# Kernel tuning notes

Hardware: AMD Instinct MI355X
Metric: run time of the kernel (lower is better)

Reference implementation:

```python
import jax, jax.numpy as jnp
import numpy as np

FEATURE_MAPS = 128
POOLING_OUT = 4
KERNAL_LEN = 3
EMB_DIM = 300
CLASSES = 7
B, L, N = 64, 512, 2048


def setup_inputs() -> dict:
    key = jax.random.key(0)
    ks = jax.random.split(key, 10)
    sentence = jax.random.normal(ks[0], (B, 1, L, EMB_DIM), dtype=jnp.float32)
    # ROIs: [x1, x2) spans within [0, L], span length in [1, 32]
    x1 = jax.random.randint(ks[1], (N,), 0, L - 33)
    span = jax.random.randint(ks[2], (N,), 1, 33)
    rois = jnp.stack([x1, x1 + span], axis=1).astype(jnp.int64)
    ridx = jax.random.randint(ks[3], (N,), 0, B).astype(jnp.int64)
    s = 0.02
    conv_w = jax.random.normal(ks[4], (FEATURE_MAPS, 1, KERNAL_LEN, EMB_DIM), dtype=jnp.float32) * s
    conv_b = jax.random.normal(ks[5], (FEATURE_MAPS,), dtype=jnp.float32) * s
    FF = FEATURE_MAPS * POOLING_OUT
    fc1_w = jax.random.normal(ks[6], (FF, FF), dtype=jnp.float32) * s
    fc1_b = jax.random.normal(ks[7], (FF,), dtype=jnp.float32) * s
    cls_w = jax.random.normal(ks[8], (CLASSES + 1, FF), dtype=jnp.float32) * s
    cls_b = jax.random.normal(ks[9], (CLASSES + 1,), dtype=jnp.float32) * s
    return {"sentence": sentence, "rois": rois, "ridx": ridx,
            "conv_w": conv_w, "conv_b": conv_b, "fc1_w": fc1_w, "fc1_b": fc1_b,
            "cls_w": cls_w, "cls_b": cls_b}


def reference(sentence, rois, ridx, conv_w, conv_b, fc1_w, fc1_b, cls_w, cls_b):
    # conv1: Conv2d(1->F, (K, D), padding=(1,0)) + ReLU -> [B, F, L, 1]
    feat = jax.lax.conv_general_dilated(
        sentence, conv_w, window_strides=(1, 1),
        padding=((1, 1), (0, 0)),
        dimension_numbers=("NCHW", "OIHW", "NCHW"))
    feat = jax.nn.relu(feat + conv_b[None, :, None, None])[..., 0]  # [B, F, L]
    # ROI max-pool over each span [x1, x2) of the length dim (vectorized)
    g = feat[ridx]                                  # [N, F, L]
    pos = jnp.arange(feat.shape[-1])
    mask = (pos[None, :] >= rois[:, 0:1]) & (pos[None, :] < rois[:, 1:2])  # [N, L]
    neg = jnp.finfo(feat.dtype).min
    pooled = jnp.max(jnp.where(mask[:, None, :], g, neg), axis=-1)  # [N, F]
    # AdaptiveMaxPool2d((1, P)) with input width 1 replicates each channel P times,
    # and .view flattening is channel-major -> jnp.repeat along last axis matches.
    x = jnp.repeat(pooled, POOLING_OUT, axis=-1)    # [N, F*P]
    x = x @ fc1_w.T + fc1_b
    return x @ cls_w.T + cls_b                      # [N, CLASSES+1]
```

## Files before the change

### kernel.cpp

```cpp
#include <hip/hip_runtime.h>
#include <hip/hip_bf16.h>

#define FMAPS 128
#define SEQL  512
#define BATCH 64
#define EMB   300
#define EMBP  320
#define LPAD  514
#define NKC   30
#define NROI  2048
#define FFDIM 512
#define NCLS  8

typedef short bf16x8 __attribute__((ext_vector_type(8)));
typedef float f32x4  __attribute__((ext_vector_type(4)));

static __device__ __forceinline__ float relu_(float x) { return x > 0.f ? x : 0.f; }
static __device__ __forceinline__ ushort bf16bits(float f) {
    __hip_bfloat16 h = __float2bfloat16(f);
    return *reinterpret_cast<ushort*>(&h);
}

__global__ void pad_bf16(const float* __restrict__ x, ushort* __restrict__ xp) {
    const int ROW4 = EMBP / 4;
    int idx = blockIdx.x * blockDim.x + threadIdx.x;
    int total = BATCH * LPAD * ROW4;
    if (idx >= total) return;
    int d4 = idx % ROW4;
    int t  = idx / ROW4;
    int r  = t % LPAD;
    int b  = t / LPAD;
    float4 v = make_float4(0.f, 0.f, 0.f, 0.f);
    if (r >= 1 && r <= SEQL && d4 < (EMB / 4)) {
        v = ((const float4*)(x + ((size_t)(b * SEQL + (r - 1))) * EMB))[d4];
    }
    ushort4 o;
    o.x = bf16bits(v.x); o.y = bf16bits(v.y); o.z = bf16bits(v.z); o.w = bf16bits(v.w);
    ((ushort4*)xp)[idx] = o;
}

__global__ void wpad_frag(const float* __restrict__ cw, ushort* __restrict__ wf) {
    int idx = blockIdx.x * blockDim.x + threadIdx.x;
    if (idx >= NKC * 8 * 64 * 8) return;
    int j    = idx & 7;
    int lane = (idx >> 3) & 63;
    int nt   = (idx >> 9) & 7;
    int kc   = idx >> 12;
    int f = nt * 16 + (lane & 15);
    int k = kc * 32 + (lane >> 4) * 8 + j;
    int kr = k / EMBP, d = k % EMBP;
    float v = (d < EMB) ? cw[f * 900 + kr * 300 + d] : 0.f;
    wf[idx] = bf16bits(v);
}

__global__ void prep_kernel(const float* __restrict__ cls_w,
                            const float* __restrict__ fc1_b,
                            const float* __restrict__ cls_b,
                            float* __restrict__ Mf, float* __restrict__ b2) {
    int t = threadIdx.x;
    Mf[t] = 0.f; Mf[t + 512] = 0.f;
    int c = t >> 6, lane = t & 63;
    float s = 0.f;
    for (int i = lane; i < FFDIM; i += 64)
        s = fmaf(cls_w[c * FFDIM + i], fc1_b[i], s);
#pragma unroll
    for (int off = 32; off; off >>= 1) s += __shfl_xor(s, off, 64);
    if (lane == 0) b2[c] = s + cls_b[c];
}

__global__ void collapse_kernel(const float* __restrict__ cls_w,
                                const float* __restrict__ fc1_w,
                                float* __restrict__ Mf) {
    int f  = threadIdx.x & 127;
    int c0 = (threadIdx.x >> 7) * 4;
    int i0 = blockIdx.x * 16;
    float acc[4] = {0.f, 0.f, 0.f, 0.f};
    for (int i = i0; i < i0 + 16; ++i) {
        float4 w4 = *(const float4*)(fc1_w + (size_t)i * FFDIM + f * 4);
        float ws = (w4.x + w4.y) + (w4.z + w4.w);
#pragma unroll
        for (int cc = 0; cc < 4; ++cc)
            acc[cc] = fmaf(cls_w[(c0 + cc) * FFDIM + i], ws, acc[cc]);
    }
#pragma unroll
    for (int cc = 0; cc < 4; ++cc)
        atomicAdd(Mf + (c0 + cc) * FMAPS + f, acc[cc]);
}

__global__ __launch_bounds__(256, 2) void conv_mfma(
    const ushort* __restrict__ xp, const ushort* __restrict__ wf,
    const float* __restrict__ cb, float* __restrict__ feat) {
    const int t    = threadIdx.x;
    const int lane = t & 63;
    const int wid  = t >> 6;
    const int wm   = wid & 1;
    const int wn   = wid >> 1;
    const int b    = blockIdx.x >> 3;
    const int l0   = (blockIdx.x & 7) << 6;

    const int mrow = lane & 15;
    const int koct = lane >> 4;

    f32x4 acc[2][4] = {};

    const ushort* xrow0 = xp + ((size_t)b * LPAD + (l0 + wm * 32 + mrow)) * EMBP + koct * 8;
    const ushort* wlane = wf + (size_t)(wn * 4) * 512 + (size_t)lane * 8;

#pragma unroll
    for (int kr = 0; kr < 3; ++kr) {
        const ushort* xr = xrow0 + (size_t)kr * EMBP;
#pragma unroll
        for (int dc = 0; dc < 10; ++dc) {
            const int kc = kr * 10 + dc;
            bf16x8 a0 = *(const bf16x8*)(xr + dc * 32);
            bf16x8 a1 = *(const bf16x8*)(xr + 16 * EMBP + dc * 32);
            const ushort* wk = wlane + (size_t)kc * 4096;
            bf16x8 b0 = *(const bf16x8*)(wk);
            bf16x8 b1 = *(const bf16x8*)(wk + 512);
            bf16x8 b2v = *(const bf16x8*)(wk + 1024);
            bf16x8 b3 = *(const bf16x8*)(wk + 1536);
            acc[0][0] = __builtin_amdgcn_mfma_f32_16x16x32_bf16(a0, b0,  acc[0][0], 0, 0, 0);
            acc[0][1] = __builtin_amdgcn_mfma_f32_16x16x32_bf16(a0, b1,  acc[0][1], 0, 0, 0);
            acc[0][2] = __builtin_amdgcn_mfma_f32_16x16x32_bf16(a0, b2v, acc[0][2], 0, 0, 0);
            acc[0][3] = __builtin_amdgcn_mfma_f32_16x16x32_bf16(a0, b3,  acc[0][3], 0, 0, 0);
            acc[1][0] = __builtin_amdgcn_mfma_f32_16x16x32_bf16(a1, b0,  acc[1][0], 0, 0, 0);
            acc[1][1] = __builtin_amdgcn_mfma_f32_16x16x32_bf16(a1, b1,  acc[1][1], 0, 0, 0);
            acc[1][2] = __builtin_amdgcn_mfma_f32_16x16x32_bf16(a1, b2v, acc[1][2], 0, 0, 0);
            acc[1][3] = __builtin_amdgcn_mfma_f32_16x16x32_bf16(a1, b3,  acc[1][3], 0, 0, 0);
        }
    }

#pragma unroll
    for (int n = 0; n < 4; ++n) {
        const int f = wn * 64 + n * 16 + mrow;
        const float bias = cb[f];
#pragma unroll
        for (int m = 0; m < 2; ++m) {
            const int lbase = l0 + wm * 32 + m * 16 + koct * 4;
#pragma unroll
            for (int r = 0; r < 4; ++r) {
                float v = acc[m][n][r] + bias;
                feat[((size_t)b * SEQL + (lbase + r)) * FMAPS + f] = relu_(v);
            }
        }
    }
}

__global__ __launch_bounds__(256) void roi_fc(
    const float* __restrict__ feat, const int* __restrict__ rois,
    const int* __restrict__ ridx, const float* __restrict__ mf,
    const float* __restrict__ b2, float* __restrict__ out) {
    const int w    = threadIdx.x >> 6;
    const int lane = threadIdx.x & 63;
    const int n    = blockIdx.x * 4 + w;
    const int x1 = rois[n * 2 + 0];
    const int x2 = rois[n * 2 + 1];
    const int bi = ridx[n];
    const float* base = feat + ((size_t)bi * SEQL) * FMAPS;
    float m0 = -1e30f, m1 = -1e30f;
    for (int l = x1; l < x2; ++l) {
        const float* row = base + (size_t)l * FMAPS;
        m0 = fmaxf(m0, row[lane]);
        m1 = fmaxf(m1, row[lane + 64]);
    }
    float res[8];
#pragma unroll
    for (int c = 0; c < 8; ++c) {
        float p = m0 * mf[c * FMAPS + lane] + m1 * mf[c * FMAPS + 64 + lane];
#pragma unroll
        for (int off = 32; off; off >>= 1) p += __shfl_xor(p, off, 64);
        res[c] = p;
    }
    if (lane == 0) {
#pragma unroll
        for (int c = 0; c < 8; ++c) out[n * NCLS + c] = res[c] + b2[c];
    }
}

extern "C" void kernel_launch(void* const* d_in, const int* in_sizes, int n_in,
                              void* d_out, int out_size, void* d_ws, size_t ws_size,
                              hipStream_t stream) {
    const float* sentence = (const float*)d_in[0];
    const int*   rois     = (const int*)d_in[1];
    const int*   ridx     = (const int*)d_in[2];
    const float* conv_w   = (const float*)d_in[3];
    const float* conv_b   = (const float*)d_in[4];
    const float* fc1_w    = (const float*)d_in[5];
    const float* fc1_b    = (const float*)d_in[6];
    const float* cls_w    = (const float*)d_in[7];
    const float* cls_b    = (const float*)d_in[8];
    float* out = (float*)d_out;

    char* ws = (char*)d_ws;
    ushort* Xp = (ushort*)ws;
    ushort* Wf = (ushort*)(ws + 21053440);
    float*  Ft = (float*)(ws + 21053440 + 245760);
    float*  Mf = (float*)(ws + 21053440 + 245760 + 16777216);
    float*  b2 = Mf + 1024;

    const int padTotal = BATCH * LPAD * (EMBP / 4);
    hipLaunchKernelGGL(pad_bf16, dim3((padTotal + 255) / 256), dim3(256), 0, stream,
                       sentence, Xp);
    hipLaunchKernelGGL(wpad_frag, dim3((NKC * 8 * 64 * 8) / 256), dim3(256), 0, stream,
                       conv_w, Wf);
    hipLaunchKernelGGL(prep_kernel, dim3(1), dim3(512), 0, stream,
                       cls_w, fc1_b, cls_b, Mf, b2);
    hipLaunchKernelGGL(collapse_kernel, dim3(32), dim3(256), 0, stream,
                       cls_w, fc1_w, Mf);
    hipLaunchKernelGGL(conv_mfma, dim3((BATCH * SEQL) / 64), dim3(256), 0, stream,
                       Xp, Wf, conv_b, Ft);
    hipLaunchKernelGGL(roi_fc, dim3(NROI / 4), dim3(256), 0, stream,
                       Ft, rois, ridx, Mf, b2, out);
}
```

Measured before the change: 140.1 us.

## Fuse preprocessing kernels into one launch and widen conv blocks to 512 threads

Merges the four preprocessing kernels (input pad/convert, weight fragment packing, fc collapse, bias fold) into one launch that dispatches on block index. The collapse step now computes each class row in a single block with a shared-memory reduction instead of zero-initialising and using atomics. The conv kernel moves to 8 waves per block, each holding a 2x2 tile of accumulators instead of 2x4, so it uses fewer registers per wave and can keep more waves resident, at the cost of more A-operand loads per MFMA.

```diff
diff --git a/kernel.cpp b/kernel.cpp
--- a/kernel.cpp
+++ b/kernel.cpp
@@ -12,6 +12,11 @@
 #define FFDIM 512
 #define NCLS  8
 
+#define PAD_BLOCKS  10280
+#define WPAD_BLOCKS 480
+#define MF_BLOCKS   8
+#define B2_BLOCKS   1
+
 typedef short bf16x8 __attribute__((ext_vector_type(8)));
 typedef float f32x4  __attribute__((ext_vector_type(4)));
 
@@ -21,90 +26,95 @@
     return *reinterpret_cast<ushort*>(&h);
 }
 
-__global__ void pad_bf16(const float* __restrict__ x, ushort* __restrict__ xp) {
-    const int ROW4 = EMBP / 4;
-    int idx = blockIdx.x * blockDim.x + threadIdx.x;
-    int total = BATCH * LPAD * ROW4;
-    if (idx >= total) return;
-    int d4 = idx % ROW4;
-    int t  = idx / ROW4;
-    int r  = t % LPAD;
-    int b  = t / LPAD;
-    float4 v = make_float4(0.f, 0.f, 0.f, 0.f);
-    if (r >= 1 && r <= SEQL && d4 < (EMB / 4)) {
-        v = ((const float4*)(x + ((size_t)(b * SEQL + (r - 1))) * EMB))[d4];
-    }
-    ushort4 o;
-    o.x = bf16bits(v.x); o.y = bf16bits(v.y); o.z = bf16bits(v.z); o.w = bf16bits(v.w);
-    ((ushort4*)xp)[idx] = o;
-}
-
-__global__ void wpad_frag(const float* __restrict__ cw, ushort* __restrict__ wf) {
-    int idx = blockIdx.x * blockDim.x + threadIdx.x;
-    if (idx >= NKC * 8 * 64 * 8) return;
-    int j    = idx & 7;
-    int lane = (idx >> 3) & 63;
-    int nt   = (idx >> 9) & 7;
-    int kc   = idx >> 12;
-    int f = nt * 16 + (lane & 15);
-    int k = kc * 32 + (lane >> 4) * 8 + j;
-    int kr = k / EMBP, d = k % EMBP;
-    float v = (d < EMB) ? cw[f * 900 + kr * 300 + d] : 0.f;
-    wf[idx] = bf16bits(v);
-}
-
-__global__ void prep_kernel(const float* __restrict__ cls_w,
-                            const float* __restrict__ fc1_b,
-                            const float* __restrict__ cls_b,
-                            float* __restrict__ Mf, float* __restrict__ b2) {
-    int t = threadIdx.x;
-    Mf[t] = 0.f; Mf[t + 512] = 0.f;
-    int c = t >> 6, lane = t & 63;
-    float s = 0.f;
-    for (int i = lane; i < FFDIM; i += 64)
-        s = fmaf(cls_w[c * FFDIM + i], fc1_b[i], s);
-#pragma unroll
-    for (int off = 32; off; off >>= 1) s += __shfl_xor(s, off, 64);
-    if (lane == 0) b2[c] = s + cls_b[c];
-}
-
-__global__ void collapse_kernel(const float* __restrict__ cls_w,
-                                const float* __restrict__ fc1_w,
-                                float* __restrict__ Mf) {
-    int f  = threadIdx.x & 127;
-    int c0 = (threadIdx.x >> 7) * 4;
-    int i0 = blockIdx.x * 16;
-    float acc[4] = {0.f, 0.f, 0.f, 0.f};
-    for (int i = i0; i < i0 + 16; ++i) {
-        float4 w4 = *(const float4*)(fc1_w + (size_t)i * FFDIM + f * 4);
-        float ws = (w4.x + w4.y) + (w4.z + w4.w);
-#pragma unroll
-        for (int cc = 0; cc < 4; ++cc)
-            acc[cc] = fmaf(cls_w[(c0 + cc) * FFDIM + i], ws, acc[cc]);
-    }
-#pragma unroll
-    for (int cc = 0; cc < 4; ++cc)
-        atomicAdd(Mf + (c0 + cc) * FMAPS + f, acc[cc]);
-}
-
-__global__ __launch_bounds__(256, 2) void conv_mfma(
+__global__ __launch_bounds__(256) void prep_fused(
+    const float* __restrict__ x, const float* __restrict__ conv_w,
+    const float* __restrict__ cls_w, const float* __restrict__ fc1_w,
+    const float* __restrict__ fc1_b, const float* __restrict__ cls_b,
+    ushort* __restrict__ xp, ushort* __restrict__ wf,
+    float* __restrict__ Mf, float* __restrict__ b2) {
+    __shared__ float red[2][128];
+    const int tid = threadIdx.x;
+    int blk = blockIdx.x;
+
+    if (blk < PAD_BLOCKS) {
+        const int ROW4 = EMBP / 4;
+        int idx = blk * 256 + tid;
+        int d4 = idx % ROW4;
+        int t  = idx / ROW4;
+        int r  = t % LPAD;
+        int b  = t / LPAD;
+        float4 v = make_float4(0.f, 0.f, 0.f, 0.f);
+        if (r >= 1 && r <= SEQL && d4 < (EMB / 4)) {
+            v = ((const float4*)(x + ((size_t)(b * SEQL + (r - 1))) * EMB))[d4];
+        }
+        ushort4 o;
+        o.x = bf16bits(v.x); o.y = bf16bits(v.y); o.z = bf16bits(v.z); o.w = bf16bits(v.w);
+        ((ushort4*)xp)[idx] = o;
+        return;
+    }
+    blk -= PAD_BLOCKS;
+
+    if (blk < WPAD_BLOCKS) {
+        int idx = blk * 256 + tid;
+        int j    = idx & 7;
+        int lane = (idx >> 3) & 63;
+        int nt   = (idx >> 9) & 7;
+        int kc   = idx >> 12;
+        int f = nt * 16 + (lane & 15);
+        int k = kc * 32 + (lane >> 4) * 8 + j;
+        int kr = k / EMBP, d = k % EMBP;
+        float v = (d < EMB) ? conv_w[f * 900 + kr * 300 + d] : 0.f;
+        wf[idx] = bf16bits(v);
+        return;
+    }
+    blk -= WPAD_BLOCKS;
+
+    if (blk < MF_BLOCKS) {
+        const int c = blk;
+        const int g = tid & 127;
+        const int q = tid >> 7;
+        float s = 0.f;
+        for (int i = q * 256; i < q * 256 + 256; ++i) {
+            float4 w4 = *(const float4*)(fc1_w + (size_t)i * FFDIM + 4 * g);
+            float ws = (w4.x + w4.y) + (w4.z + w4.w);
+            s = fmaf(cls_w[c * FFDIM + i], ws, s);
+        }
+        red[q][g] = s;
+        __syncthreads();
+        if (tid < 128) Mf[c * FMAPS + tid] = red[0][tid] + red[1][tid];
+        return;
+    }
+
+    {
+        const int c = tid >> 5;
+        const int l32 = tid & 31;
+        float s = 0.f;
+        for (int i = l32; i < FFDIM; i += 32)
+            s = fmaf(cls_w[c * FFDIM + i], fc1_b[i], s);
+#pragma unroll
+        for (int off = 16; off; off >>= 1) s += __shfl_xor(s, off, 64);
+        if (l32 == 0) b2[c] = s + cls_b[c];
+    }
+}
+
+__global__ __launch_bounds__(512, 4) void conv_mfma(
     const ushort* __restrict__ xp, const ushort* __restrict__ wf,
     const float* __restrict__ cb, float* __restrict__ feat) {
     const int t    = threadIdx.x;
     const int lane = t & 63;
     const int wid  = t >> 6;
-    const int wm   = wid & 1;
-    const int wn   = wid >> 1;
+    const int wm   = wid >> 2;
+    const int wn   = wid & 3;
     const int b    = blockIdx.x >> 3;
     const int l0   = (blockIdx.x & 7) << 6;
 
     const int mrow = lane & 15;
     const int koct = lane >> 4;
 
-    f32x4 acc[2][4] = {};
+    f32x4 acc[2][2] = {};
 
     const ushort* xrow0 = xp + ((size_t)b * LPAD + (l0 + wm * 32 + mrow)) * EMBP + koct * 8;
-    const ushort* wlane = wf + (size_t)(wn * 4) * 512 + (size_t)lane * 8;
+    const ushort* wlane = wf + (size_t)(wn * 2) * 512 + (size_t)lane * 8;
 
 #pragma unroll
     for (int kr = 0; kr < 3; ++kr) {
@@ -117,22 +127,16 @@
             const ushort* wk = wlane + (size_t)kc * 4096;
             bf16x8 b0 = *(const bf16x8*)(wk);
             bf16x8 b1 = *(const bf16x8*)(wk + 512);
-            bf16x8 b2v = *(const bf16x8*)(wk + 1024);
-            bf16x8 b3 = *(const bf16x8*)(wk + 1536);
-            acc[0][0] = __builtin_amdgcn_mfma_f32_16x16x32_bf16(a0, b0,  acc[0][0], 0, 0, 0);
-            acc[0][1] = __builtin_amdgcn_mfma_f32_16x16x32_bf16(a0, b1,  acc[0][1], 0, 0, 0);
-            acc[0][2] = __builtin_amdgcn_mfma_f32_16x16x32_bf16(a0, b2v, acc[0][2], 0, 0, 0);
-            acc[0][3] = __builtin_amdgcn_mfma_f32_16x16x32_bf16(a0, b3,  acc[0][3], 0, 0, 0);
-            acc[1][0] = __builtin_amdgcn_mfma_f32_16x16x32_bf16(a1, b0,  acc[1][0], 0, 0, 0);
-            acc[1][1] = __builtin_amdgcn_mfma_f32_16x16x32_bf16(a1, b1,  acc[1][1], 0, 0, 0);
-            acc[1][2] = __builtin_amdgcn_mfma_f32_16x16x32_bf16(a1, b2v, acc[1][2], 0, 0, 0);
-            acc[1][3] = __builtin_amdgcn_mfma_f32_16x16x32_bf16(a1, b3,  acc[1][3], 0, 0, 0);
-        }
-    }
-
-#pragma unroll
-    for (int n = 0; n < 4; ++n) {
-        const int f = wn * 64 + n * 16 + mrow;
+            acc[0][0] = __builtin_amdgcn_mfma_f32_16x16x32_bf16(a0, b0, acc[0][0], 0, 0, 0);
+            acc[0][1] = __builtin_amdgcn_mfma_f32_16x16x32_bf16(a0, b1, acc[0][1], 0, 0, 0);
+            acc[1][0] = __builtin_amdgcn_mfma_f32_16x16x32_bf16(a1, b0, acc[1][0], 0, 0, 0);
+            acc[1][1] = __builtin_amdgcn_mfma_f32_16x16x32_bf16(a1, b1, acc[1][1], 0, 0, 0);
+        }
+    }
+
+#pragma unroll
+    for (int n = 0; n < 2; ++n) {
+        const int f = wn * 32 + n * 16 + mrow;
         const float bias = cb[f];
 #pragma unroll
         for (int m = 0; m < 2; ++m) {
@@ -198,16 +202,10 @@
     float*  Mf = (float*)(ws + 21053440 + 245760 + 16777216);
     float*  b2 = Mf + 1024;
 
-    const int padTotal = BATCH * LPAD * (EMBP / 4);
-    hipLaunchKernelGGL(pad_bf16, dim3((padTotal + 255) / 256), dim3(256), 0, stream,
-                       sentence, Xp);
-    hipLaunchKernelGGL(wpad_frag, dim3((NKC * 8 * 64 * 8) / 256), dim3(256), 0, stream,
-                       conv_w, Wf);
-    hipLaunchKernelGGL(prep_kernel, dim3(1), dim3(512), 0, stream,
-                       cls_w, fc1_b, cls_b, Mf, b2);
-    hipLaunchKernelGGL(collapse_kernel, dim3(32), dim3(256), 0, stream,
-                       cls_w, fc1_w, Mf);
-    hipLaunchKernelGGL(conv_mfma, dim3((BATCH * SEQL) / 64), dim3(256), 0, stream,
+    hipLaunchKernelGGL(prep_fused,
+                       dim3(PAD_BLOCKS + WPAD_BLOCKS + MF_BLOCKS + B2_BLOCKS), dim3(256), 0, stream,
+                       sentence, conv_w, cls_w, fc1_w, fc1_b, cls_b, Xp, Wf, Mf, b2);
+    hipLaunchKernelGGL(conv_mfma, dim3((BATCH * SEQL) / 64), dim3(512), 0, stream,
                        Xp, Wf, conv_b, Ft);
     hipLaunchKernelGGL(roi_fc, dim3(NROI / 4), dim3(256), 0, stream,
                        Ft, rois, ridx, Mf, b2, out);
```

After: 156.6 us. 11.8% more time.
